# Kernel optimization log

Hardware: AMD Instinct MI355X
Metric: run time of the kernel (lower is better)

Reference implementation:

```python
import jax, jax.numpy as jnp
import numpy as np

NEG_SLOPE = 0.2  # PyG GATConv default


def gat_conv(x, edge_index, W, att_src, att_dst, bias, heads, out_c, concat):
    """One PyG-style GATConv layer (eval mode, add_self_loops=True)."""
    N = x.shape[0]
    loop = jnp.arange(N, dtype=edge_index.dtype)
    src = jnp.concatenate([edge_index[0], loop])  # [E+N]
    dst = jnp.concatenate([edge_index[1], loop])
    h = (x @ W).reshape(N, heads, out_c)                     # [N,H,C]
    a_src = jnp.einsum('nhc,hc->nh', h, att_src)             # [N,H]
    a_dst = jnp.einsum('nhc,hc->nh', h, att_dst)
    e = jax.nn.leaky_relu(a_src[src] + a_dst[dst], NEG_SLOPE)  # [E+N,H]
    # segment softmax over incoming edges of each dst node (self-loops guarantee non-empty segments)
    emax = jax.ops.segment_max(e, dst, num_segments=N)
    e = jnp.exp(e - emax[dst])
    denom = jax.ops.segment_sum(e, dst, num_segments=N)
    alpha = e / denom[dst]                                   # [E+N,H]
    msg = h[src] * alpha[:, :, None]                         # [E+N,H,C]
    out = jax.ops.segment_sum(msg, dst, num_segments=N)      # [N,H,C]
    out = out.reshape(N, heads * out_c) if concat else out.mean(axis=1)
    return out + bias


def setup_inputs() -> dict:
    key = jax.random.key(0)
    ks = jax.random.split(key, 10)
    N, E, Fin, Hc, H, Out = 20000, 320000, 256, 128, 4, 256
    s = lambda k, shp: jax.random.normal(k, shp, dtype=jnp.float32) * 0.05
    return {
        'x': jax.random.normal(ks[0], (N, Fin), dtype=jnp.float32),
        'edge_index': jax.random.randint(ks[1], (2, E), 0, N, dtype=jnp.int64),
        'W1': s(ks[2], (Fin, H * Hc)),
        'att_src1': s(ks[3], (H, Hc)),
        'att_dst1': s(ks[4], (H, Hc)),
        'b1': s(ks[5], (H * Hc,)),
        'W2': s(ks[6], (H * Hc, Out)),
        'att_src2': s(ks[7], (1, Out)),
        'att_dst2': s(ks[8], (1, Out)),
        'b2': s(ks[9], (Out,)),
    }


def reference(x, edge_index, W1, att_src1, att_dst1, b1, W2, att_src2, att_dst2, b2):
    h = gat_conv(x, edge_index, W1, att_src1, att_dst1, b1, heads=4, out_c=128, concat=True)
    h = jax.nn.gelu(h, approximate=False)  # torch.nn.GELU default is exact
    out = gat_conv(h, edge_index, W2, att_src2, att_dst2, b2, heads=1, out_c=256, concat=False)
    return out
```

## Files before the change

kernel.cpp:

```cpp
#include <hip/hip_runtime.h>
#include <hip/hip_bf16.h>

#define NODES 20000
#define EDGES 320000
#define FIN   256
#define HEADS 4
#define C1    128
#define F1    512
#define F2    256
#define TOT_E (EDGES + NODES)

typedef __bf16 bf16x8 __attribute__((ext_vector_type(8)));
typedef float  f32x4  __attribute__((ext_vector_type(4)));
typedef unsigned short ushort_t;
typedef ushort_t ushx8 __attribute__((ext_vector_type(8)));

#define GLOAD_LDS16(gp, lp) \
    __builtin_amdgcn_global_load_lds((const __attribute__((address_space(1))) void*)(gp), \
                                     (__attribute__((address_space(3))) void*)(lp), 16, 0, 0)

__device__ __forceinline__ float bf2f(ushort_t u) {
    union { unsigned int i; float f; } c; c.i = ((unsigned)u) << 16; return c.f;
}
__device__ __forceinline__ ushort_t f2bf(float f) {
    union { float f; unsigned int i; } c; c.f = f;
    unsigned r = (c.i + 0x7fffu + ((c.i >> 16) & 1u)) >> 16;
    return (ushort_t)r;
}
__device__ __forceinline__ float lrelu(float v) { return (v > 0.f) ? v : 0.2f * v; }

#define CAST_T (NODES * FIN / 4)
#define T1N    (FIN * F1)
#define T2N    (F1 * F2)
__global__ void k_prep(const float* __restrict__ x, ushort_t* __restrict__ x_bf,
                       const float* __restrict__ W1, ushort_t* __restrict__ w1t,
                       const float* __restrict__ W2, ushort_t* __restrict__ w2t) {
    int t = blockIdx.x * 256 + threadIdx.x;
    if (t < CAST_T) {
        int i = t * 4;
        float4 v = *reinterpret_cast<const float4*>(x + i);
        ushort4 o;
        o.x = f2bf(v.x); o.y = f2bf(v.y); o.z = f2bf(v.z); o.w = f2bf(v.w);
        *reinterpret_cast<ushort4*>(x_bf + i) = o;
    } else if (t < CAST_T + T1N) {
        int idx = t - CAST_T;
        int n = idx >> 8, k = idx & 255;
        w1t[idx] = f2bf(W1[k * F1 + n]);
    } else if (t < CAST_T + T1N + T2N) {
        int idx = t - CAST_T - T1N;
        int n = idx >> 9, k = idx & 511;
        w2t[idx] = f2bf(W2[k * F2 + n]);
    }
}

__global__ void k_hist(const int* __restrict__ ei, int* __restrict__ counts) {
    int e = blockIdx.x * blockDim.x + threadIdx.x;
    if (e >= TOT_E) return;
    int dst = (e < EDGES) ? ei[EDGES + e] : (e - EDGES);
    atomicAdd(&counts[dst], 1);
}

__global__ void k_scan(const int* __restrict__ counts, int* __restrict__ offsets, int* __restrict__ cursor) {
    __shared__ int wsum[16];
    const int PT = 20;
    int tid = threadIdx.x;
    int lane = tid & 63, wv = tid >> 6;
    int base = tid * PT;
    int v[PT];
    int tsum = 0;
    #pragma unroll
    for (int i = 0; i < PT; i++) {
        int idx = base + i;
        v[i] = (idx < NODES) ? counts[idx] : 0;
        tsum += v[i];
    }
    int orig = tsum;
    for (int o = 1; o < 64; o <<= 1) {
        int t = __shfl_up(tsum, o);
        if (lane >= o) tsum += t;
    }
    if (lane == 63) wsum[wv] = tsum;
    __syncthreads();
    if (wv == 0 && lane < 16) {
        int s = wsum[lane];
        for (int o = 1; o < 16; o <<= 1) {
            int t = __shfl_up(s, o);
            if (lane >= o) s += t;
        }
        wsum[lane] = s;
    }
    __syncthreads();
    int wpre = (wv == 0) ? 0 : wsum[wv - 1];
    int excl = wpre + tsum - orig;
    #pragma unroll
    for (int i = 0; i < PT; i++) {
        int idx = base + i;
        if (idx < NODES) { offsets[idx] = excl; cursor[idx] = excl; }
        excl += v[i];
    }
}

__global__ void k_scatter(const int* __restrict__ ei, int* __restrict__ cursor, int* __restrict__ csr_src) {
    int e = blockIdx.x * blockDim.x + threadIdx.x;
    if (e >= TOT_E) return;
    int src, dst;
    if (e < EDGES) { src = ei[e]; dst = ei[EDGES + e]; }
    else           { src = dst = e - EDGES; }
    int pos = atomicAdd(&cursor[dst], 1);
    csr_src[pos] = src;
}

__launch_bounds__(256)
__global__ void k_gemm_att(const ushort_t* __restrict__ A, const ushort_t* __restrict__ Bt,
                           ushort_t* __restrict__ Cbf, int M, int N, int K,
                           const float* __restrict__ attS, const float* __restrict__ attD,
                           float* __restrict__ aS, float* __restrict__ aD, int aStride) {
    __shared__ ushort_t lA[128 * 64];
    __shared__ ushort_t lB[128 * 64];
    const int tid  = threadIdx.x;
    const int lane = tid & 63, w = tid >> 6;
    const int wr = w >> 1, wc = w & 1;
    const int row0 = blockIdx.x * 128;
    const int col0 = blockIdx.y * 128;
    f32x4 acc[4][4] = {};

    const int srow = lane >> 3;
    const int scol = (lane & 7) * 8;

    for (int k0 = 0; k0 < K; k0 += 64) {
        #pragma unroll
        for (int p = 0; p < 4; p++) {
            int rb = p * 32 + w * 8;
            GLOAD_LDS16(&A[(size_t)(row0 + rb + srow) * K + k0 + scol], &lA[rb * 64]);
            GLOAD_LDS16(&Bt[(size_t)(col0 + rb + srow) * K + k0 + scol], &lB[rb * 64]);
        }
        __syncthreads();
        #pragma unroll
        for (int kk = 0; kk < 2; kk++) {
            int kb = kk * 32 + (lane >> 4) * 8;
            bf16x8 af[4], bfr[4];
            #pragma unroll
            for (int m = 0; m < 4; m++)
                af[m] = *reinterpret_cast<const bf16x8*>(&lA[(wr * 64 + m * 16 + (lane & 15)) * 64 + kb]);
            #pragma unroll
            for (int n = 0; n < 4; n++)
                bfr[n] = *reinterpret_cast<const bf16x8*>(&lB[(wc * 64 + n * 16 + (lane & 15)) * 64 + kb]);
            #pragma unroll
            for (int m = 0; m < 4; m++)
                #pragma unroll
                for (int n = 0; n < 4; n++)
                    acc[m][n] = __builtin_amdgcn_mfma_f32_16x16x32_bf16(af[m], bfr[n], acc[m][n], 0, 0, 0);
        }
        __syncthreads();
    }

    #pragma unroll
    for (int m = 0; m < 4; m++) {
        int gr0 = row0 + wr * 64 + m * 16 + (lane >> 4) * 4;
        #pragma unroll
        for (int n = 0; n < 4; n++) {
            int gc = col0 + wc * 64 + n * 16 + (lane & 15);
            #pragma unroll
            for (int r = 0; r < 4; r++) {
                int gr = gr0 + r;
                if (gr < M) Cbf[(size_t)gr * N + gc] = f2bf(acc[m][n][r]);
            }
        }
    }

    float pds[16], pdd[16];
    #pragma unroll
    for (int i = 0; i < 16; i++) { pds[i] = 0.f; pdd[i] = 0.f; }
    const int attBase = blockIdx.y * 128;
    #pragma unroll
    for (int n = 0; n < 4; n++) {
        int colr = wc * 64 + n * 16 + (lane & 15);
        float av = attS[attBase + colr];
        float dv = attD[attBase + colr];
        #pragma unroll
        for (int m = 0; m < 4; m++)
            #pragma unroll
            for (int r = 0; r < 4; r++) {
                pds[m * 4 + r] += acc[m][n][r] * av;
                pdd[m * 4 + r] += acc[m][n][r] * dv;
            }
    }
    #pragma unroll
    for (int o = 1; o < 16; o <<= 1) {
        #pragma unroll
        for (int i = 0; i < 16; i++) {
            pds[i] += __shfl_xor(pds[i], o);
            pdd[i] += __shfl_xor(pdd[i], o);
        }
    }
    if ((lane & 15) == 0) {
        int hoff = (aStride == HEADS) ? blockIdx.y : 0;
        #pragma unroll
        for (int m = 0; m < 4; m++)
            #pragma unroll
            for (int r = 0; r < 4; r++) {
                int gr = row0 + wr * 64 + m * 16 + (lane >> 4) * 4 + r;
                if (gr < M) {
                    atomicAdd(&aS[gr * aStride + hoff], pds[m * 4 + r]);
                    atomicAdd(&aD[gr * aStride + hoff], pdd[m * 4 + r]);
                }
            }
    }
}

__launch_bounds__(256)
__global__ void k_agg1(const ushort_t* __restrict__ h1, const int* __restrict__ offsets,
                       const int* __restrict__ counts, const int* __restrict__ csr,
                       const float* __restrict__ a_src, const float* __restrict__ a_dst,
                       const float* __restrict__ b1, ushort_t* __restrict__ hgelu) {
    int w = threadIdx.x >> 6, lane = threadIdx.x & 63;
    int d = blockIdx.x * 4 + w;
    int h = lane >> 4;
    int off = offsets[d], deg = counts[d];
    float adst = a_dst[d * HEADS + h];
    float acc[8] = {};
    float den = 0.f;
    int j = 0;
    for (; j + 4 <= deg; j += 4) {
        int s0 = csr[off + j + 0];
        int s1 = csr[off + j + 1];
        int s2 = csr[off + j + 2];
        int s3 = csr[off + j + 3];
        ushx8 v0 = *reinterpret_cast<const ushx8*>(&h1[(size_t)s0 * F1 + lane * 8]);
        ushx8 v1 = *reinterpret_cast<const ushx8*>(&h1[(size_t)s1 * F1 + lane * 8]);
        ushx8 v2 = *reinterpret_cast<const ushx8*>(&h1[(size_t)s2 * F1 + lane * 8]);
        ushx8 v3 = *reinterpret_cast<const ushx8*>(&h1[(size_t)s3 * F1 + lane * 8]);
        float w0 = __expf(lrelu(a_src[s0 * HEADS + h] + adst));
        float w1 = __expf(lrelu(a_src[s1 * HEADS + h] + adst));
        float w2 = __expf(lrelu(a_src[s2 * HEADS + h] + adst));
        float w3 = __expf(lrelu(a_src[s3 * HEADS + h] + adst));
        den += (w0 + w1) + (w2 + w3);
        #pragma unroll
        for (int i = 0; i < 8; i++)
            acc[i] += w0 * bf2f(v0[i]) + w1 * bf2f(v1[i]) + w2 * bf2f(v2[i]) + w3 * bf2f(v3[i]);
    }
    for (; j < deg; j++) {
        int s = csr[off + j];
        ushx8 hv = *reinterpret_cast<const ushx8*>(&h1[(size_t)s * F1 + lane * 8]);
        float wgt = __expf(lrelu(a_src[s * HEADS + h] + adst));
        den += wgt;
        #pragma unroll
        for (int i = 0; i < 8; i++) acc[i] += wgt * bf2f(hv[i]);
    }
    float inv = 1.f / den;
    int c0 = lane * 8;
    ushx8 o;
    #pragma unroll
    for (int i = 0; i < 8; i++) {
        float v = acc[i] * inv + b1[c0 + i];
        v = 0.5f * v * (1.f + erff(v * 0.70710678118654752f));
        o[i] = f2bf(v);
    }
    *reinterpret_cast<ushx8*>(&hgelu[(size_t)d * F1 + c0]) = o;
}

__launch_bounds__(256)
__global__ void k_agg2(const ushort_t* __restrict__ h2, const int* __restrict__ offsets,
                       const int* __restrict__ counts, const int* __restrict__ csr,
                       const float* __restrict__ a_src, const float* __restrict__ a_dst,
                       const float* __restrict__ b2, float* __restrict__ out) {
    int w = threadIdx.x >> 6, lane = threadIdx.x & 63;
    int d = blockIdx.x * 4 + w;
    int off = offsets[d], deg = counts[d];
    int half = lane >> 5, il = lane & 31;
    float adst = a_dst[d];
    float acc[8] = {};
    float den = 0.f;
    int j = 0;
    for (; j + 8 <= deg; j += 8) {
        int s0 = csr[off + j + 0 + half];
        int s1 = csr[off + j + 2 + half];
        int s2 = csr[off + j + 4 + half];
        int s3 = csr[off + j + 6 + half];
        ushx8 v0 = *reinterpret_cast<const ushx8*>(&h2[(size_t)s0 * F2 + il * 8]);
        ushx8 v1 = *reinterpret_cast<const ushx8*>(&h2[(size_t)s1 * F2 + il * 8]);
        ushx8 v2 = *reinterpret_cast<const ushx8*>(&h2[(size_t)s2 * F2 + il * 8]);
        ushx8 v3 = *reinterpret_cast<const ushx8*>(&h2[(size_t)s3 * F2 + il * 8]);
        float w0 = __expf(lrelu(a_src[s0] + adst));
        float w1 = __expf(lrelu(a_src[s1] + adst));
        float w2 = __expf(lrelu(a_src[s2] + adst));
        float w3 = __expf(lrelu(a_src[s3] + adst));
        den += (w0 + w1) + (w2 + w3);
        #pragma unroll
        for (int i = 0; i < 8; i++)
            acc[i] += w0 * bf2f(v0[i]) + w1 * bf2f(v1[i]) + w2 * bf2f(v2[i]) + w3 * bf2f(v3[i]);
    }
    for (; j < deg; j += 2) {
        int jj = j + half;
        if (jj < deg) {
            int s = csr[off + jj];
            ushx8 hv = *reinterpret_cast<const ushx8*>(&h2[(size_t)s * F2 + il * 8]);
            float wgt = __expf(lrelu(a_src[s] + adst));
            den += wgt;
            #pragma unroll
            for (int i = 0; i < 8; i++) acc[i] += wgt * bf2f(hv[i]);
        }
    }
    den += __shfl_xor(den, 32);
    #pragma unroll
    for (int i = 0; i < 8; i++) acc[i] += __shfl_xor(acc[i], 32);
    if (half == 0) {
        float inv = 1.f / den;
        int c0 = il * 8;
        float4 o0, o1;
        o0.x = acc[0] * inv + b2[c0 + 0];
        o0.y = acc[1] * inv + b2[c0 + 1];
        o0.z = acc[2] * inv + b2[c0 + 2];
        o0.w = acc[3] * inv + b2[c0 + 3];
        o1.x = acc[4] * inv + b2[c0 + 4];
        o1.y = acc[5] * inv + b2[c0 + 5];
        o1.z = acc[6] * inv + b2[c0 + 6];
        o1.w = acc[7] * inv + b2[c0 + 7];
        *reinterpret_cast<float4*>(&out[(size_t)d * F2 + c0])     = o0;
        *reinterpret_cast<float4*>(&out[(size_t)d * F2 + c0 + 4]) = o1;
    }
}

extern "C" void kernel_launch(void* const* d_in, const int* in_sizes, int n_in,
                              void* d_out, int out_size, void* d_ws, size_t ws_size,
                              hipStream_t stream) {
    const float* x        = (const float*)d_in[0];
    const int*   ei       = (const int*)d_in[1];
    const float* W1       = (const float*)d_in[2];
    const float* att_src1 = (const float*)d_in[3];
    const float* att_dst1 = (const float*)d_in[4];
    const float* b1       = (const float*)d_in[5];
    const float* W2       = (const float*)d_in[6];
    const float* att_src2 = (const float*)d_in[7];
    const float* att_dst2 = (const float*)d_in[8];
    const float* b2       = (const float*)d_in[9];
    float* out = (float*)d_out;

    char* p = (char*)d_ws;
    auto alloc = [&](size_t bytes) -> char* {
        char* r = p; p += (bytes + 255) & ~(size_t)255; return r;
    };
    ushort_t* x_bf  = (ushort_t*)alloc((size_t)NODES * FIN * 2);
    ushort_t* w1t   = (ushort_t*)alloc((size_t)F1 * FIN * 2);
    ushort_t* w2t   = (ushort_t*)alloc((size_t)F2 * F1 * 2);
    ushort_t* h1    = (ushort_t*)alloc((size_t)NODES * F1 * 2);
    ushort_t* hg    = (ushort_t*)alloc((size_t)NODES * F1 * 2);
    ushort_t* h2    = (ushort_t*)alloc((size_t)NODES * F2 * 2);
    char* zbase     = p;
    int* counts     = (int*)alloc((size_t)NODES * 4);
    float* as1      = (float*)alloc((size_t)NODES * HEADS * 4);
    float* ad1      = (float*)alloc((size_t)NODES * HEADS * 4);
    float* as2      = (float*)alloc((size_t)NODES * 4);
    float* ad2      = (float*)alloc((size_t)NODES * 4);
    size_t zspan    = (size_t)(p - zbase);
    int* offsets    = (int*)alloc((size_t)NODES * 4);
    int* cursor     = (int*)alloc((size_t)NODES * 4);
    int* csr        = (int*)alloc((size_t)TOT_E * 4);

    hipMemsetAsync(zbase, 0, zspan, stream);
    k_prep<<<(CAST_T + T1N + T2N + 255) / 256, 256, 0, stream>>>(x, x_bf, W1, w1t, W2, w2t);
    k_hist<<<(TOT_E + 255) / 256, 256, 0, stream>>>(ei, counts);
    k_scan<<<1, 1024, 0, stream>>>(counts, offsets, cursor);
    k_scatter<<<(TOT_E + 255) / 256, 256, 0, stream>>>(ei, cursor, csr);

    k_gemm_att<<<dim3(157, 4), 256, 0, stream>>>(x_bf, w1t, h1, NODES, F1, FIN,
                                                 att_src1, att_dst1, as1, ad1, HEADS);
    k_agg1<<<NODES / 4, 256, 0, stream>>>(h1, offsets, counts, csr, as1, ad1, b1, hg);

    k_gemm_att<<<dim3(157, 2), 256, 0, stream>>>(hg, w2t, h2, NODES, F2, F1,
                                                 att_src2, att_dst2, as2, ad2, 1);
    k_agg2<<<NODES / 4, 256, 0, stream>>>(h2, offsets, counts, csr, as2, ad2, b2, out);
}
```

Before: 289.1 us.

## Precompute layer-2 attention vectors via W2·att and swizzle GEMM LDS layout

Folds the layer-2 attention projections into precomputed vectors W2·att_src2 and W2·att_dst2, so the per-node a_src2/a_dst2 scores are computed as dot products in the agg1 epilogue. This removes the atomic reduction from the second GEMM. The histogram kernel is merged into the prep kernel, and the GEMM's LDS tiles get an XOR swizzle to cut bank conflicts. h2 reuses the x_bf buffer, and the layer-2 attention buffers no longer need zeroing. The scores are now computed from the bf16 GELU output and fp32 weights rather than the bf16 GEMM accumulators, which slightly changes rounding.

After: 306.4 us. 6.0% more time.

```diff
diff --git a/kernel.cpp b/kernel.cpp
--- a/kernel.cpp
+++ b/kernel.cpp
@@ -32,9 +32,13 @@
 #define CAST_T (NODES * FIN / 4)
 #define T1N    (FIN * F1)
 #define T2N    (F1 * F2)
+#define PREP_T (CAST_T + T1N + T2N + 512 + TOT_E)
 __global__ void k_prep(const float* __restrict__ x, ushort_t* __restrict__ x_bf,
                        const float* __restrict__ W1, ushort_t* __restrict__ w1t,
-                       const float* __restrict__ W2, ushort_t* __restrict__ w2t) {
+                       const float* __restrict__ W2, ushort_t* __restrict__ w2t,
+                       const float* __restrict__ attS2, const float* __restrict__ attD2,
+                       float* __restrict__ w2s, float* __restrict__ w2d,
+                       const int* __restrict__ ei, int* __restrict__ counts) {
     int t = blockIdx.x * 256 + threadIdx.x;
     if (t < CAST_T) {
         int i = t * 4;
@@ -50,14 +54,17 @@
         int idx = t - CAST_T - T1N;
         int n = idx >> 9, k = idx & 511;
         w2t[idx] = f2bf(W2[k * F2 + n]);
-    }
-}
-
-__global__ void k_hist(const int* __restrict__ ei, int* __restrict__ counts) {
-    int e = blockIdx.x * blockDim.x + threadIdx.x;
-    if (e >= TOT_E) return;
-    int dst = (e < EDGES) ? ei[EDGES + e] : (e - EDGES);
-    atomicAdd(&counts[dst], 1);
+    } else if (t < CAST_T + T1N + T2N + 512) {
+        int f = t - CAST_T - T1N - T2N;
+        const float* row = W2 + (size_t)f * F2;
+        float s = 0.f, d = 0.f;
+        for (int o = 0; o < F2; o++) { float v = row[o]; s += v * attS2[o]; d += v * attD2[o]; }
+        w2s[f] = s; w2d[f] = d;
+    } else if (t < PREP_T) {
+        int e = t - CAST_T - T1N - T2N - 512;
+        int dst = (e < EDGES) ? ei[EDGES + e] : (e - EDGES);
+        atomicAdd(&counts[dst], 1);
+    }
 }
 
 __global__ void k_scan(const int* __restrict__ counts, int* __restrict__ offsets, int* __restrict__ cursor) {
@@ -114,7 +121,8 @@
 __global__ void k_gemm_att(const ushort_t* __restrict__ A, const ushort_t* __restrict__ Bt,
                            ushort_t* __restrict__ Cbf, int M, int N, int K,
                            const float* __restrict__ attS, const float* __restrict__ attD,
-                           float* __restrict__ aS, float* __restrict__ aD, int aStride) {
+                           float* __restrict__ aS, float* __restrict__ aD, int aStride,
+                           int doAtt) {
     __shared__ ushort_t lA[128 * 64];
     __shared__ ushort_t lB[128 * 64];
     const int tid  = threadIdx.x;
@@ -125,7 +133,7 @@
     f32x4 acc[4][4] = {};
 
     const int srow = lane >> 3;
-    const int scol = (lane & 7) * 8;
+    const int scol = ((lane & 7) ^ srow) * 8;
 
     for (int k0 = 0; k0 < K; k0 += 64) {
         #pragma unroll
@@ -137,14 +145,15 @@
         __syncthreads();
         #pragma unroll
         for (int kk = 0; kk < 2; kk++) {
-            int kb = kk * 32 + (lane >> 4) * 8;
+            const int q = lane >> 4;
+            const int sw = ((kk * 4 + q) ^ (lane & 7)) * 8;
             bf16x8 af[4], bfr[4];
             #pragma unroll
             for (int m = 0; m < 4; m++)
-                af[m] = *reinterpret_cast<const bf16x8*>(&lA[(wr * 64 + m * 16 + (lane & 15)) * 64 + kb]);
+                af[m] = *reinterpret_cast<const bf16x8*>(&lA[(wr * 64 + m * 16 + (lane & 15)) * 64 + sw]);
             #pragma unroll
             for (int n = 0; n < 4; n++)
-                bfr[n] = *reinterpret_cast<const bf16x8*>(&lB[(wc * 64 + n * 16 + (lane & 15)) * 64 + kb]);
+                bfr[n] = *reinterpret_cast<const bf16x8*>(&lB[(wc * 64 + n * 16 + (lane & 15)) * 64 + sw]);
             #pragma unroll
             for (int m = 0; m < 4; m++)
                 #pragma unroll
@@ -168,6 +177,7 @@
         }
     }
 
+    if (!doAtt) return;
     float pds[16], pdd[16];
     #pragma unroll
     for (int i = 0; i < 16; i++) { pds[i] = 0.f; pdd[i] = 0.f; }
@@ -194,7 +204,7 @@
         }
     }
     if ((lane & 15) == 0) {
-        int hoff = (aStride == HEADS) ? blockIdx.y : 0;
+        int hoff = blockIdx.y;
         #pragma unroll
         for (int m = 0; m < 4; m++)
             #pragma unroll
@@ -212,7 +222,9 @@
 __global__ void k_agg1(const ushort_t* __restrict__ h1, const int* __restrict__ offsets,
                        const int* __restrict__ counts, const int* __restrict__ csr,
                        const float* __restrict__ a_src, const float* __restrict__ a_dst,
-                       const float* __restrict__ b1, ushort_t* __restrict__ hgelu) {
+                       const float* __restrict__ b1, ushort_t* __restrict__ hgelu,
+                       const float* __restrict__ w2s, const float* __restrict__ w2d,
+                       float* __restrict__ as2, float* __restrict__ ad2) {
     int w = threadIdx.x >> 6, lane = threadIdx.x & 63;
     int d = blockIdx.x * 4 + w;
     int h = lane >> 4;
@@ -250,13 +262,20 @@
     float inv = 1.f / den;
     int c0 = lane * 8;
     ushx8 o;
+    float ds2 = 0.f, dd2 = 0.f;
     #pragma unroll
     for (int i = 0; i < 8; i++) {
         float v = acc[i] * inv + b1[c0 + i];
         v = 0.5f * v * (1.f + erff(v * 0.70710678118654752f));
         o[i] = f2bf(v);
+        float vb = bf2f(o[i]);
+        ds2 += vb * w2s[c0 + i];
+        dd2 += vb * w2d[c0 + i];
     }
     *reinterpret_cast<ushx8*>(&hgelu[(size_t)d * F1 + c0]) = o;
+    #pragma unroll
+    for (int q = 1; q < 64; q <<= 1) { ds2 += __shfl_xor(ds2, q); dd2 += __shfl_xor(dd2, q); }
+    if (lane == 0) { as2[d] = ds2; ad2[d] = dd2; }
 }
 
 __launch_bounds__(256)
@@ -345,29 +364,32 @@
     ushort_t* w2t   = (ushort_t*)alloc((size_t)F2 * F1 * 2);
     ushort_t* h1    = (ushort_t*)alloc((size_t)NODES * F1 * 2);
     ushort_t* hg    = (ushort_t*)alloc((size_t)NODES * F1 * 2);
-    ushort_t* h2    = (ushort_t*)alloc((size_t)NODES * F2 * 2);
+    ushort_t* h2    = x_bf;
     char* zbase     = p;
     int* counts     = (int*)alloc((size_t)NODES * 4);
     float* as1      = (float*)alloc((size_t)NODES * HEADS * 4);
     float* ad1      = (float*)alloc((size_t)NODES * HEADS * 4);
+    size_t zspan    = (size_t)(p - zbase);
     float* as2      = (float*)alloc((size_t)NODES * 4);
     float* ad2      = (float*)alloc((size_t)NODES * 4);
-    size_t zspan    = (size_t)(p - zbase);
+    float* w2s      = (float*)alloc((size_t)F1 * 4);
+    float* w2d      = (float*)alloc((size_t)F1 * 4);
     int* offsets    = (int*)alloc((size_t)NODES * 4);
     int* cursor     = (int*)alloc((size_t)NODES * 4);
     int* csr        = (int*)alloc((size_t)TOT_E * 4);
 
     hipMemsetAsync(zbase, 0, zspan, stream);
-    k_prep<<<(CAST_T + T1N + T2N + 255) / 256, 256, 0, stream>>>(x, x_bf, W1, w1t, W2, w2t);
-    k_hist<<<(TOT_E + 255) / 256, 256, 0, stream>>>(ei, counts);
+    k_prep<<<(PREP_T + 255) / 256, 256, 0, stream>>>(x, x_bf, W1, w1t, W2, w2t,
+                                                     att_src2, att_dst2, w2s, w2d,
+                                                     ei, counts);
     k_scan<<<1, 1024, 0, stream>>>(counts, offsets, cursor);
     k_scatter<<<(TOT_E + 255) / 256, 256, 0, stream>>>(ei, cursor, csr);
 
     k_gemm_att<<<dim3(157, 4), 256, 0, stream>>>(x_bf, w1t, h1, NODES, F1, FIN,
-                                                 att_src1, att_dst1, as1, ad1, HEADS);
-    k_agg1<<<NODES / 4, 256, 0, stream>>>(h1, offsets, counts, csr, as1, ad1, b1, hg);
-
+                                                 att_src1, att_dst1, as1, ad1, HEADS, 1);
+    k_agg1<<<NODES / 4, 256, 0, stream>>>(h1, offsets, counts, csr, as1, ad1, b1, hg,
+                                          w2s, w2d, as2, ad2);
     k_gemm_att<<<dim3(157, 2), 256, 0, stream>>>(hg, w2t, h2, NODES, F2, F1,
-                                                 att_src2, att_dst2, as2, ad2, 1);
+                                                 nullptr, nullptr, nullptr, nullptr, 1, 0);
     k_agg2<<<NODES / 4, 256, 0, stream>>>(h2, offsets, counts, csr, as2, ad2, b2, out);
 }
```
